# Kernel optimization log

Hardware: AMD Instinct MI355X
Metric: run time of the kernel (lower is better)

Reference implementation:

```python
import jax, jax.numpy as jnp
import numpy as np

N, L, P = 8192, 20, 30          # obstacles, observation_len, pred_len
E, H, C = 64, 128, 2048         # embed_size, hidden_size, cnn_out_size (resnet50)


def setup_inputs() -> dict:
    key = jax.random.key(0)
    ks = jax.random.split(key, 10)
    rn = lambda k, s, sc=1.0: jax.random.normal(k, s, jnp.float32) * sc
    return {
        "img_embedding": rn(ks[0], (N, C)),
        "obs_pos": rn(ks[1], (N, L, 2)),
        "obs_pos_rel": rn(ks[2], (N, L, 2), 0.1),
        "obs_hist_size": jax.random.randint(ks[3], (N,), 0, L, jnp.int32),
        "h0": rn(ks[4], (H,), 0.1),
        "W_embed": rn(ks[5], (2, E), 0.5),
        "b_embed": jnp.zeros((E,), jnp.float32),
        "W_ih": rn(ks[6], (E, 4 * H), 1.0 / np.sqrt(E)),
        "W_hh": rn(ks[7], (H, 4 * H), 1.0 / np.sqrt(H)),
        "b_ih": jnp.zeros((4 * H,), jnp.float32),
        "b_hh": jnp.zeros((4 * H,), jnp.float32),
        "W_pred": rn(ks[8], (H + C, 2), 1.0 / np.sqrt(H + C)),
        "b_pred": jnp.zeros((2,), jnp.float32),
    }


def _forward(img_embedding, obs_pos, obs_pos_rel, obs_hist_size, h0,
             W_embed, b_embed, W_ih, W_hh, b_ih, b_hh, W_pred, b_pred):
    n, l, _ = obs_pos.shape
    hid = h0.shape[0]
    h = jnp.broadcast_to(h0, (n, hid))
    c = h  # original code initializes BOTH ht and ct from h0 (faithful to source)

    def lstm_cell(h, c, rel):
        # disp_embed (Linear(2,E)+ReLU) followed by a single LSTM step, PyTorch gate order i,f,g,o
        e = jax.nn.relu(rel @ W_embed + b_embed)            # [n, E]
        g = e @ W_ih + h @ W_hh + (b_ih + b_hh)             # [n, 4H]
        i, f, gg, o = jnp.split(g, 4, axis=-1)
        c_new = jax.nn.sigmoid(f) * c + jax.nn.sigmoid(i) * jnp.tanh(gg)
        h_new = jax.nn.sigmoid(o) * jnp.tanh(c_new)
        return h_new, c_new

    # ---- observation phase: t = 1 .. l-1, masked state update ----
    thresh = l - jnp.arange(1, l)                           # [l-1]
    masks = obs_hist_size[None, :] > thresh[:, None]        # [l-1, n] bool
    rels = jnp.swapaxes(obs_pos_rel[:, 1:, :], 0, 1)        # [l-1, n, 2]

    def obs_step(carry, x):
        h, c = carry
        rel, m = x
        h_new, c_new = lstm_cell(h, c, rel)
        m = m[:, None]
        return (jnp.where(m, h_new, h), jnp.where(m, c_new, c)), None

    (h, c), _ = jax.lax.scan(obs_step, (h, c), (rels, masks))

    # ---- prediction phase: pred_mask == all ones ----
    # pred_layer(cat(ht, img_emb)) == ht @ Wp_h + (img_emb @ Wp_img + b); the image
    # part is loop-invariant so hoist it (same math, far less memory traffic).
    img_proj = img_embedding @ W_pred[hid:] + b_pred        # [n, 2]
    Wp_h = W_pred[:hid]                                     # [H, 2]

    def pred_step(carry, _):
        h, c, pos = carry
        rel = h @ Wp_h + img_proj                           # pred_out[:, t-L]
        pos = pos + rel                                     # pred_traj[:, t-L]
        h_new, c_new = lstm_cell(h, c, rel)
        return (h_new, c_new, pos), pos

    _, traj = jax.lax.scan(pred_step, (h, c, obs_pos[:, -1, :]), None, length=P)
    return jnp.swapaxes(traj, 0, 1)                         # [n, P, 2]


def reference(img_embedding, obs_pos, obs_pos_rel, obs_hist_size, h0,
              W_embed, b_embed, W_ih, W_hh, b_ih, b_hh, W_pred, b_pred):
    return _forward(img_embedding, obs_pos, obs_pos_rel, obs_hist_size, h0,
                    W_embed, b_embed, W_ih, W_hh, b_ih, b_hh, W_pred, b_pred)
```

## Files before the change

### kernel.cpp

```cpp
#include <hip/hip_runtime.h>

typedef float f32x4 __attribute__((ext_vector_type(4)));
typedef float f32x2 __attribute__((ext_vector_type(2)));
typedef short bf16x8 __attribute__((ext_vector_type(8)));
typedef short short4v __attribute__((ext_vector_type(4)));

#define N_TOT 8192
#define L_OBS 20
#define P_PRED 30
#define E_DIM 64
#define H_DIM 128
#define C_DIM 2048
#define G_DIM 512
#define M_ROWS 32
#define NTH 512
#define A_PAD 200

#define K1 1.442695041f
#define K2 2.885390082f

static __device__ __forceinline__ unsigned short f2bf(float f) {
  union { float f; unsigned int u; } v; v.f = f;
  unsigned int u = v.u;
  return (unsigned short)((u + 0x7FFFu + ((u >> 16) & 1u)) >> 16);
}
static __device__ __forceinline__ float bf2f(unsigned short b) {
  union { unsigned int u; float f; } v; v.u = ((unsigned int)b) << 16;
  return v.f;
}
static __device__ __forceinline__ float ex2(float x)  { float r; asm("v_exp_f32 %0, %1" : "=v"(r) : "v"(x)); return r; }
static __device__ __forceinline__ float rcpn(float x) { float r; asm("v_rcp_f32 %0, %1" : "=v"(r) : "v"(x)); return r; }

__global__ __launch_bounds__(NTH, 2)
void lstm_traj(const float* __restrict__ img,
               const float* __restrict__ obs_pos,
               const float* __restrict__ obs_rel,
               const int*   __restrict__ hist,
               const float* __restrict__ h0,
               const float* __restrict__ W_embed,
               const float* __restrict__ b_embed,
               const float* __restrict__ W_ih,
               const float* __restrict__ W_hh,
               const float* __restrict__ b_ih,
               const float* __restrict__ b_hh,
               const float* __restrict__ W_pred,
               const float* __restrict__ b_pred,
               float* __restrict__ out)
{
  __shared__ unsigned short A_lds[2][M_ROWS][A_PAD];
  __shared__ float We_lds[2][E_DIM];
  __shared__ float be_lds[E_DIM];
  __shared__ float Wp_lds[H_DIM][2];

  const int t    = threadIdx.x;
  const int w    = t >> 6;
  const int l    = t & 63;
  const int u15  = l & 15;
  const int rq   = l >> 4;
  const int u    = w * 16 + u15;
  const int wg0  = blockIdx.x * M_ROWS;
  const int grow = t >> 4;
  const int gj   = t & 15;

  if (t < 128) We_lds[t >> 6][t & 63] = W_embed[t];
  if (t < 64)  be_lds[t] = b_embed[t];
  if (t >= 128 && t < 384) ((float*)Wp_lds)[t - 128] = W_pred[t - 128];
  __syncthreads();

  bf16x8 B[4][6];
#pragma unroll
  for (int ks = 0; ks < 6; ++ks)
#pragma unroll
    for (int i = 0; i < 8; ++i) {
      const int k = ks * 32 + rq * 8 + i;
      const float* Wrow = (k < E_DIM) ? (W_ih + k * G_DIM) : (W_hh + (k - E_DIM) * G_DIM);
#pragma unroll
      for (int gt = 0; gt < 4; ++gt)
        B[gt][ks][i] = (short)f2bf(Wrow[gt * 128 + u]);
    }

  const float nbi = -K1 * (b_ih[u]       + b_hh[u]);
  const float nbf = -K1 * (b_ih[128 + u] + b_hh[128 + u]);
  const float nbg = -K2 * (b_ih[256 + u] + b_hh[256 + u]);
  const float nbo = -K1 * (b_ih[384 + u] + b_hh[384 + u]);

  const float h0u = h0[u];
  const unsigned short h0b = f2bf(h0u);
  unsigned short hb[2][4];
  float cs[2][4];
  int sact[2];
#pragma unroll
  for (int rt = 0; rt < 2; ++rt) {
    sact[rt] = 0;
#pragma unroll
    for (int q = 0; q < 4; ++q) {
      const int row = rt * 16 + rq * 4 + q;
      hb[rt][q] = h0b; cs[rt][q] = h0u;
      sact[rt] |= ((20 - hist[wg0 + row]) & 255) << (8 * q);
      A_lds[0][row][64 + u] = h0b;
    }
  }

  {
    const f32x2 rr = *(const f32x2*)(obs_rel + (wg0 + grow) * (L_OBS * 2) + 2 * 2);
    short4v ep;
#pragma unroll
    for (int i = 0; i < 4; ++i) {
      const int j = gj * 4 + i;
      float e = fmaf(rr.x, We_lds[0][j], fmaf(rr.y, We_lds[1][j], be_lds[j]));
      ep[i] = (short)f2bf(fmaxf(e, 0.0f));
    }
    *(short4v*)&A_lds[0][grow][gj * 4] = ep;
  }

  float pos0 = obs_pos[(wg0 + grow) * (L_OBS * 2) + (L_OBS - 1) * 2];
  float pos1 = obs_pos[(wg0 + grow) * (L_OBS * 2) + (L_OBS - 1) * 2 + 1];
  float ip0 = 0.f, ip1 = 0.f;
  {
    const float* irow = img + (long)(wg0 + grow) * C_DIM;
#pragma unroll 4
    for (int i = 0; i < 32; ++i) {
      const int k0 = i * 64 + gj * 4;
      const f32x4 v  = *(const f32x4*)(irow + k0);
      const f32x4 wa = *(const f32x4*)(W_pred + (H_DIM + k0) * 2);
      const f32x4 wb = *(const f32x4*)(W_pred + (H_DIM + k0) * 2 + 4);
      ip0 = fmaf(v.x, wa.x, fmaf(v.y, wa.z, fmaf(v.z, wb.x, fmaf(v.w, wb.z, ip0))));
      ip1 = fmaf(v.x, wa.y, fmaf(v.y, wa.w, fmaf(v.z, wb.y, fmaf(v.w, wb.w, ip1))));
    }
#pragma unroll
    for (int m = 8; m >= 1; m >>= 1) { ip0 += __shfl_xor(ip0, m); ip1 += __shfl_xor(ip1, m); }
    ip0 += b_pred[0]; ip1 += b_pred[1];
  }
  __syncthreads();

  int cur = 0;

  auto lstm_step = [&](int cur_, int nxt_, int s_, bool domask) {
    f32x4 acc[2][4];
#pragma unroll
    for (int rt = 0; rt < 2; ++rt) {
#pragma unroll
      for (int gt = 0; gt < 4; ++gt) { acc[rt][gt].x = 0.f; acc[rt][gt].y = 0.f; acc[rt][gt].z = 0.f; acc[rt][gt].w = 0.f; }
#pragma unroll
      for (int ks = 0; ks < 6; ++ks) {
        const bf16x8 a = *(const bf16x8*)&A_lds[cur_][rt * 16 + u15][ks * 32 + rq * 8];
#pragma unroll
        for (int gt = 0; gt < 4; ++gt)
          acc[rt][gt] = __builtin_amdgcn_mfma_f32_16x16x32_bf16(a, B[gt][ks], acc[rt][gt], 0, 0, 0);
      }
    }
#pragma unroll
    for (int rt = 0; rt < 2; ++rt)
#pragma unroll
      for (int q = 0; q < 4; ++q) {
        const float si = rcpn(1.f + ex2(fmaf(acc[rt][0][q], -K1, nbi)));
        const float sf = rcpn(1.f + ex2(fmaf(acc[rt][1][q], -K1, nbf)));
        const float tg = fmaf(2.f, rcpn(1.f + ex2(fmaf(acc[rt][2][q], -K2, nbg))), -1.f);
        const float so = rcpn(1.f + ex2(fmaf(acc[rt][3][q], -K1, nbo)));
        const float cn = fmaf(sf, cs[rt][q], si * tg);
        const float tc = fmaf(2.f, rcpn(1.f + ex2(-K2 * cn)), -1.f);
        const float hn = so * tc;
        bool act = true;
        if (domask) act = s_ >= ((sact[rt] >> (8 * q)) & 255);
        if (act) { cs[rt][q] = cn; hb[rt][q] = f2bf(hn); }
        A_lds[nxt_][rt * 16 + rq * 4 + q][64 + u] = hb[rt][q];
      }
  };

#pragma unroll 1
  for (int s = 1; s < L_OBS - 1; ++s) {
    const int nxt = cur ^ 1;
    f32x2 rrN;
    const bool havN = (s + 2) <= (L_OBS - 1);
    if (havN) rrN = *(const f32x2*)(obs_rel + (wg0 + grow) * (L_OBS * 2) + (s + 2) * 2);
    lstm_step(cur, nxt, s, true);
    if (havN) {
      short4v ep;
#pragma unroll
      for (int i = 0; i < 4; ++i) {
        const int j = gj * 4 + i;
        float e = fmaf(rrN.x, We_lds[0][j], fmaf(rrN.y, We_lds[1][j], be_lds[j]));
        ep[i] = (short)f2bf(fmaxf(e, 0.0f));
      }
      *(short4v*)&A_lds[nxt][grow][gj * 4] = ep;
    }
    cur = nxt;
    __syncthreads();
  }

#pragma unroll 1
  for (int p = 0; p < P_PRED; ++p) {
    const bf16x8 hv = *(const bf16x8*)&A_lds[cur][grow][64 + gj * 8];
    float s0 = 0.f, s1 = 0.f;
#pragma unroll
    for (int i = 0; i < 8; ++i) {
      const float hf = bf2f((unsigned short)hv[i]);
      s0 = fmaf(hf, Wp_lds[gj * 8 + i][0], s0);
      s1 = fmaf(hf, Wp_lds[gj * 8 + i][1], s1);
    }
#pragma unroll
    for (int m = 8; m >= 1; m >>= 1) { s0 += __shfl_xor(s0, m); s1 += __shfl_xor(s1, m); }
    const float rel0 = s0 + ip0, rel1 = s1 + ip1;
    pos0 += rel0; pos1 += rel1;
    if (gj == 0) {
      float2 o; o.x = pos0; o.y = pos1;
      *(float2*)&out[((long)(wg0 + grow) * P_PRED + p) * 2] = o;
    }
    if (p == P_PRED - 1) break;

    {
      short4v ep;
#pragma unroll
      for (int i = 0; i < 4; ++i) {
        const int j = gj * 4 + i;
        float e = fmaf(rel0, We_lds[0][j], fmaf(rel1, We_lds[1][j], be_lds[j]));
        ep[i] = (short)f2bf(fmaxf(e, 0.0f));
      }
      *(short4v*)&A_lds[cur][grow][gj * 4] = ep;
    }
    __syncthreads();

    const int nxt = cur ^ 1;
    lstm_step(cur, nxt, 0, false);
    cur = nxt;
    __syncthreads();
  }
}

extern "C" void kernel_launch(void* const* d_in, const int* in_sizes, int n_in,
                              void* d_out, int out_size, void* d_ws, size_t ws_size,
                              hipStream_t stream) {
  (void)in_sizes; (void)n_in; (void)out_size; (void)d_ws; (void)ws_size;
  lstm_traj<<<dim3(N_TOT / M_ROWS), dim3(NTH), 0, stream>>>(
      (const float*)d_in[0],
      (const float*)d_in[1],
      (const float*)d_in[2],
      (const int*)  d_in[3],
      (const float*)d_in[4],
      (const float*)d_in[5],
      (const float*)d_in[6],
      (const float*)d_in[7],
      (const float*)d_in[8],
      (const float*)d_in[9],
      (const float*)d_in[10],
      (const float*)d_in[11],
      (const float*)d_in[12],
      (float*)d_out);
}
```

Before: 128.8 us.

## Overlap hidden-state MFMAs with prediction output and fuse gate reciprocals

In the prediction loop, the MFMAs over the hidden-state part of K are now issued before the output projection and embedding work. Only the embedding slice is multiplied after the barrier, which shortens the serial chain per step. The gate math is rewritten to merge the sigmoid/tanh reciprocals into fewer rcp calls, and bf16 packing uses the hardware v_cvt_pk_bf16_f32 instruction instead of manual rounding. The obs-loop embedding load is made unconditional with a clamped index, and the MFMA loop order is interleaved across row tiles. The merged-reciprocal form may overflow when the exponent terms are large, which risks precision.

```diff
diff --git a/kernel.cpp b/kernel.cpp
--- a/kernel.cpp
+++ b/kernel.cpp
@@ -3,7 +3,6 @@
 typedef float f32x4 __attribute__((ext_vector_type(4)));
 typedef float f32x2 __attribute__((ext_vector_type(2)));
 typedef short bf16x8 __attribute__((ext_vector_type(8)));
-typedef short short4v __attribute__((ext_vector_type(4)));
 
 #define N_TOT 8192
 #define L_OBS 20
@@ -30,6 +29,9 @@
 }
 static __device__ __forceinline__ float ex2(float x)  { float r; asm("v_exp_f32 %0, %1" : "=v"(r) : "v"(x)); return r; }
 static __device__ __forceinline__ float rcpn(float x) { float r; asm("v_rcp_f32 %0, %1" : "=v"(r) : "v"(x)); return r; }
+static __device__ __forceinline__ unsigned int cvtpk(float lo, float hi) {
+  unsigned int r; asm("v_cvt_pk_bf16_f32 %0, %1, %2" : "=v"(r) : "v"(lo), "v"(hi)); return r;
+}
 
 __global__ __launch_bounds__(NTH, 2)
 void lstm_traj(const float* __restrict__ img,
@@ -62,6 +64,8 @@
   const int grow = t >> 4;
   const int gj   = t & 15;
 
+  const float* relrow = obs_rel + (wg0 + grow) * (L_OBS * 2);
+
   if (t < 128) We_lds[t >> 6][t & 63] = W_embed[t];
   if (t < 64)  be_lds[t] = b_embed[t];
   if (t >= 128 && t < 384) ((float*)Wp_lds)[t - 128] = W_pred[t - 128];
@@ -86,7 +90,7 @@
 
   const float h0u = h0[u];
   const unsigned short h0b = f2bf(h0u);
-  unsigned short hb[2][4];
+  float hf[2][4];
   float cs[2][4];
   int sact[2];
 #pragma unroll
@@ -95,22 +99,21 @@
 #pragma unroll
     for (int q = 0; q < 4; ++q) {
       const int row = rt * 16 + rq * 4 + q;
-      hb[rt][q] = h0b; cs[rt][q] = h0u;
+      hf[rt][q] = h0u; cs[rt][q] = h0u;
       sact[rt] |= ((20 - hist[wg0 + row]) & 255) << (8 * q);
       A_lds[0][row][64 + u] = h0b;
     }
   }
 
   {
-    const f32x2 rr = *(const f32x2*)(obs_rel + (wg0 + grow) * (L_OBS * 2) + 2 * 2);
-    short4v ep;
-#pragma unroll
-    for (int i = 0; i < 4; ++i) {
-      const int j = gj * 4 + i;
-      float e = fmaf(rr.x, We_lds[0][j], fmaf(rr.y, We_lds[1][j], be_lds[j]));
-      ep[i] = (short)f2bf(fmaxf(e, 0.0f));
-    }
-    *(short4v*)&A_lds[0][grow][gj * 4] = ep;
+    const f32x2 rr = *(const f32x2*)(relrow + 2 * 2);
+    const int j = gj * 4;
+    const float e0 = fmaxf(fmaf(rr.x, We_lds[0][j],     fmaf(rr.y, We_lds[1][j],     be_lds[j])),     0.f);
+    const float e1 = fmaxf(fmaf(rr.x, We_lds[0][j + 1], fmaf(rr.y, We_lds[1][j + 1], be_lds[j + 1])), 0.f);
+    const float e2 = fmaxf(fmaf(rr.x, We_lds[0][j + 2], fmaf(rr.y, We_lds[1][j + 2], be_lds[j + 2])), 0.f);
+    const float e3 = fmaxf(fmaf(rr.x, We_lds[0][j + 3], fmaf(rr.y, We_lds[1][j + 3], be_lds[j + 3])), 0.f);
+    uint2 pk; pk.x = cvtpk(e0, e1); pk.y = cvtpk(e2, e3);
+    *(uint2*)&A_lds[0][grow][j] = pk;
   }
 
   float pos0 = obs_pos[(wg0 + grow) * (L_OBS * 2) + (L_OBS - 1) * 2];
@@ -135,68 +138,99 @@
 
   int cur = 0;
 
-  auto lstm_step = [&](int cur_, int nxt_, int s_, bool domask) {
+  auto gates_and_h = [&](f32x4 (&acc)[2][4], int nxt_, int s_, bool domask) {
+#pragma unroll
+    for (int rt = 0; rt < 2; ++rt) {
+#pragma unroll
+      for (int q = 0; q < 4; ++q) {
+        const float A_ = ex2(fmaf(acc[rt][0][q], -K1, nbi));
+        const float F_ = ex2(fmaf(acc[rt][1][q], -K1, nbf));
+        const float B_ = ex2(fmaf(acc[rt][2][q], -K2, nbg));
+        const float C_ = ex2(fmaf(acc[rt][3][q], -K1, nbo));
+        const float P2 = 1.f + B_;
+        const float PB = (1.f + A_) * P2;
+        const float Q  = 1.f + F_;
+        const float cn = fmaf(cs[rt][q], PB, (2.f - P2) * Q) * rcpn(PB * Q);
+        const float D_ = ex2(-K2 * cn);
+        const float tc = fmaf(2.f, rcpn(1.f + D_), -1.f);
+        const float hn = tc * rcpn(1.f + C_);
+        bool act = true;
+        if (domask) act = s_ >= ((sact[rt] >> (8 * q)) & 255);
+        if (act) { cs[rt][q] = cn; hf[rt][q] = hn; }
+      }
+      const unsigned int p01 = cvtpk(hf[rt][0], hf[rt][1]);
+      const unsigned int p23 = cvtpk(hf[rt][2], hf[rt][3]);
+      const int rowb = rt * 16 + rq * 4;
+      A_lds[nxt_][rowb + 0][64 + u] = (unsigned short)p01;
+      A_lds[nxt_][rowb + 1][64 + u] = (unsigned short)(p01 >> 16);
+      A_lds[nxt_][rowb + 2][64 + u] = (unsigned short)p23;
+      A_lds[nxt_][rowb + 3][64 + u] = (unsigned short)(p23 >> 16);
+    }
+  };
+
+#pragma unroll 1
+  for (int s = 1; s < L_OBS - 1; ++s) {
+    const int nxt = cur ^ 1;
+    const int sN = (s + 2 <= L_OBS - 1) ? (s + 2) : (L_OBS - 1);
+    const f32x2 rrN = *(const f32x2*)(relrow + sN * 2);
+
     f32x4 acc[2][4];
 #pragma unroll
-    for (int rt = 0; rt < 2; ++rt) {
+    for (int rt = 0; rt < 2; ++rt)
 #pragma unroll
       for (int gt = 0; gt < 4; ++gt) { acc[rt][gt].x = 0.f; acc[rt][gt].y = 0.f; acc[rt][gt].z = 0.f; acc[rt][gt].w = 0.f; }
 #pragma unroll
-      for (int ks = 0; ks < 6; ++ks) {
-        const bf16x8 a = *(const bf16x8*)&A_lds[cur_][rt * 16 + u15][ks * 32 + rq * 8];
+    for (int ks = 0; ks < 6; ++ks)
+#pragma unroll
+      for (int rt = 0; rt < 2; ++rt) {
+        const bf16x8 a = *(const bf16x8*)&A_lds[cur][rt * 16 + u15][ks * 32 + rq * 8];
 #pragma unroll
         for (int gt = 0; gt < 4; ++gt)
           acc[rt][gt] = __builtin_amdgcn_mfma_f32_16x16x32_bf16(a, B[gt][ks], acc[rt][gt], 0, 0, 0);
       }
-    }
-#pragma unroll
-    for (int rt = 0; rt < 2; ++rt)
-#pragma unroll
-      for (int q = 0; q < 4; ++q) {
-        const float si = rcpn(1.f + ex2(fmaf(acc[rt][0][q], -K1, nbi)));
-        const float sf = rcpn(1.f + ex2(fmaf(acc[rt][1][q], -K1, nbf)));
-        const float tg = fmaf(2.f, rcpn(1.f + ex2(fmaf(acc[rt][2][q], -K2, nbg))), -1.f);
-        const float so = rcpn(1.f + ex2(fmaf(acc[rt][3][q], -K1, nbo)));
-        const float cn = fmaf(sf, cs[rt][q], si * tg);
-        const float tc = fmaf(2.f, rcpn(1.f + ex2(-K2 * cn)), -1.f);
-        const float hn = so * tc;
-        bool act = true;
-        if (domask) act = s_ >= ((sact[rt] >> (8 * q)) & 255);
-        if (act) { cs[rt][q] = cn; hb[rt][q] = f2bf(hn); }
-        A_lds[nxt_][rt * 16 + rq * 4 + q][64 + u] = hb[rt][q];
-      }
-  };
-
-#pragma unroll 1
-  for (int s = 1; s < L_OBS - 1; ++s) {
-    const int nxt = cur ^ 1;
-    f32x2 rrN;
-    const bool havN = (s + 2) <= (L_OBS - 1);
-    if (havN) rrN = *(const f32x2*)(obs_rel + (wg0 + grow) * (L_OBS * 2) + (s + 2) * 2);
-    lstm_step(cur, nxt, s, true);
-    if (havN) {
-      short4v ep;
-#pragma unroll
-      for (int i = 0; i < 4; ++i) {
-        const int j = gj * 4 + i;
-        float e = fmaf(rrN.x, We_lds[0][j], fmaf(rrN.y, We_lds[1][j], be_lds[j]));
-        ep[i] = (short)f2bf(fmaxf(e, 0.0f));
-      }
-      *(short4v*)&A_lds[nxt][grow][gj * 4] = ep;
-    }
+
+    {
+      const int j = gj * 4;
+      const float e0 = fmaxf(fmaf(rrN.x, We_lds[0][j],     fmaf(rrN.y, We_lds[1][j],     be_lds[j])),     0.f);
+      const float e1 = fmaxf(fmaf(rrN.x, We_lds[0][j + 1], fmaf(rrN.y, We_lds[1][j + 1], be_lds[j + 1])), 0.f);
+      const float e2 = fmaxf(fmaf(rrN.x, We_lds[0][j + 2], fmaf(rrN.y, We_lds[1][j + 2], be_lds[j + 2])), 0.f);
+      const float e3 = fmaxf(fmaf(rrN.x, We_lds[0][j + 3], fmaf(rrN.y, We_lds[1][j + 3], be_lds[j + 3])), 0.f);
+      uint2 pk; pk.x = cvtpk(e0, e1); pk.y = cvtpk(e2, e3);
+      *(uint2*)&A_lds[nxt][grow][j] = pk;
+    }
+
+    gates_and_h(acc, nxt, s, true);
     cur = nxt;
     __syncthreads();
   }
 
 #pragma unroll 1
   for (int p = 0; p < P_PRED; ++p) {
+    f32x4 acc[2][4];
+    const bool last = (p == P_PRED - 1);
+    if (!last) {
+#pragma unroll
+      for (int rt = 0; rt < 2; ++rt)
+#pragma unroll
+        for (int gt = 0; gt < 4; ++gt) { acc[rt][gt].x = 0.f; acc[rt][gt].y = 0.f; acc[rt][gt].z = 0.f; acc[rt][gt].w = 0.f; }
+#pragma unroll
+      for (int ks = 2; ks < 6; ++ks)
+#pragma unroll
+        for (int rt = 0; rt < 2; ++rt) {
+          const bf16x8 a = *(const bf16x8*)&A_lds[cur][rt * 16 + u15][ks * 32 + rq * 8];
+#pragma unroll
+          for (int gt = 0; gt < 4; ++gt)
+            acc[rt][gt] = __builtin_amdgcn_mfma_f32_16x16x32_bf16(a, B[gt][ks], acc[rt][gt], 0, 0, 0);
+        }
+    }
+
     const bf16x8 hv = *(const bf16x8*)&A_lds[cur][grow][64 + gj * 8];
     float s0 = 0.f, s1 = 0.f;
 #pragma unroll
     for (int i = 0; i < 8; ++i) {
-      const float hf = bf2f((unsigned short)hv[i]);
-      s0 = fmaf(hf, Wp_lds[gj * 8 + i][0], s0);
-      s1 = fmaf(hf, Wp_lds[gj * 8 + i][1], s1);
+      const float hfv = bf2f((unsigned short)hv[i]);
+      s0 = fmaf(hfv, Wp_lds[gj * 8 + i][0], s0);
+      s1 = fmaf(hfv, Wp_lds[gj * 8 + i][1], s1);
     }
 #pragma unroll
     for (int m = 8; m >= 1; m >>= 1) { s0 += __shfl_xor(s0, m); s1 += __shfl_xor(s1, m); }
@@ -206,22 +240,31 @@
       float2 o; o.x = pos0; o.y = pos1;
       *(float2*)&out[((long)(wg0 + grow) * P_PRED + p) * 2] = o;
     }
-    if (p == P_PRED - 1) break;
+    if (last) break;
 
     {
-      short4v ep;
-#pragma unroll
-      for (int i = 0; i < 4; ++i) {
-        const int j = gj * 4 + i;
-        float e = fmaf(rel0, We_lds[0][j], fmaf(rel1, We_lds[1][j], be_lds[j]));
-        ep[i] = (short)f2bf(fmaxf(e, 0.0f));
+      const int j = gj * 4;
+      const float e0 = fmaxf(fmaf(rel0, We_lds[0][j],     fmaf(rel1, We_lds[1][j],     be_lds[j])),     0.f);
+      const float e1 = fmaxf(fmaf(rel0, We_lds[0][j + 1], fmaf(rel1, We_lds[1][j + 1], be_lds[j + 1])), 0.f);
+      const float e2 = fmaxf(fmaf(rel0, We_lds[0][j + 2], fmaf(rel1, We_lds[1][j + 2], be_lds[j + 2])), 0.f);
+      const float e3 = fmaxf(fmaf(rel0, We_lds[0][j + 3], fmaf(rel1, We_lds[1][j + 3], be_lds[j + 3])), 0.f);
+      uint2 pk; pk.x = cvtpk(e0, e1); pk.y = cvtpk(e2, e3);
+      *(uint2*)&A_lds[cur][grow][j] = pk;
+    }
+    __syncthreads();
+
+#pragma unroll
+    for (int ks = 0; ks < 2; ++ks)
+#pragma unroll
+      for (int rt = 0; rt < 2; ++rt) {
+        const bf16x8 a = *(const bf16x8*)&A_lds[cur][rt * 16 + u15][ks * 32 + rq * 8];
+#pragma unroll
+        for (int gt = 0; gt < 4; ++gt)
+          acc[rt][gt] = __builtin_amdgcn_mfma_f32_16x16x32_bf16(a, B[gt][ks], acc[rt][gt], 0, 0, 0);
       }
-      *(short4v*)&A_lds[cur][grow][gj * 4] = ep;
-    }
-    __syncthreads();
 
     const int nxt = cur ^ 1;
-    lstm_step(cur, nxt, 0, false);
+    gates_and_h(acc, nxt, 0, false);
     cur = nxt;
     __syncthreads();
   }
```

Measured after the change: 125.0 us. -2.9%, faster.
